# Optimization experiments

Hardware: AMD Instinct MI355X
Metric: run time of the kernel (lower is better)

Reference implementation:

```python
import jax, jax.numpy as jnp
import numpy as np

NUM_PROTOTYPES_PER_CLASS = 4
BATCH = 16384
NUM_CLASSES = 1000


def setup_inputs() -> dict:
    key = jax.random.key(0)
    k1, k2 = jax.random.split(key)
    batch_distances = jax.random.uniform(k1, (BATCH, NUM_CLASSES * NUM_PROTOTYPES_PER_CLASS), dtype=jnp.float32)
    labels = jax.random.randint(k2, (BATCH,), 0, NUM_CLASSES, dtype=jnp.int64)
    return {"batch_distances": batch_distances, "labels": labels}


def reference(batch_distances, labels):
    B, NP = batch_distances.shape
    P = NUM_PROTOTYPES_PER_CLASS
    C = NP // P
    # (B, C, P) -> soft-min over prototypes per class
    d = -jax.nn.logsumexp(-batch_distances.reshape(B, C, P), axis=2)  # (B, C)
    in_cls = jnp.take_along_axis(d, labels[:, None], axis=1)[:, 0]    # (B,)
    # leave-one-out mean over the other C-1 classes
    out_mean = (jnp.sum(d, axis=1) - in_cls) / (C - 1)                # (B,)
    loss = jnp.mean((in_cls * in_cls) / (out_mean * out_mean))
    return loss
```

## Files before the change

### kernel.cpp

```cpp
#include <hip/hip_runtime.h>

constexpr int BATCH   = 16384;
constexpr int NCLS    = 1000;
constexpr int PROTO   = 4;
constexpr int THREADS = 256;

__global__ __launch_bounds__(THREADS)
void mpl_row_kernel(const float* __restrict__ dist,
                    const int*   __restrict__ labels,
                    float*       __restrict__ terms) {
    const int row = blockIdx.x;
    const float4* __restrict__ rp =
        reinterpret_cast<const float4*>(dist + (size_t)row * (NCLS * PROTO));
    const int lab = labels[row];
    const int t   = threadIdx.x;

    float sum   = 0.0f;
    float incls = 0.0f;
    bool  have  = false;

    for (int c = t; c < NCLS; c += THREADS) {
        float4 v = rp[c];
        float m = fminf(fminf(v.x, v.y), fminf(v.z, v.w));
        float s = expf(m - v.x) + expf(m - v.y) + expf(m - v.z) + expf(m - v.w);
        float d = m - logf(s);
        sum += d;
        if (c == lab) { incls = d; have = true; }
    }

    #pragma unroll
    for (int off = 32; off; off >>= 1) sum += __shfl_down(sum, off, 64);

    __shared__ float s_wave[THREADS / 64];
    __shared__ float s_in;
    const int lane = t & 63, wid = t >> 6;
    if (lane == 0) s_wave[wid] = sum;
    if (have)      s_in = incls;
    __syncthreads();

    if (t == 0) {
        float total = s_wave[0] + s_wave[1] + s_wave[2] + s_wave[3];
        float ic    = s_in;
        float om    = (total - ic) * (1.0f / (NCLS - 1));
        terms[row]  = (ic * ic) / (om * om);
    }
}

__global__ __launch_bounds__(THREADS)
void mpl_reduce_kernel(const float* __restrict__ terms,
                       float*       __restrict__ out) {
    const int t = threadIdx.x;
    const float4* __restrict__ tp = reinterpret_cast<const float4*>(terms);
    float sum = 0.0f;
    for (int i = t; i < BATCH / 4; i += THREADS) {
        float4 v = tp[i];
        sum += (v.x + v.y) + (v.z + v.w);
    }
    #pragma unroll
    for (int off = 32; off; off >>= 1) sum += __shfl_down(sum, off, 64);

    __shared__ float s_wave[THREADS / 64];
    const int lane = t & 63, wid = t >> 6;
    if (lane == 0) s_wave[wid] = sum;
    __syncthreads();
    if (t == 0) {
        out[0] = (s_wave[0] + s_wave[1] + s_wave[2] + s_wave[3]) * (1.0f / BATCH);
    }
}

extern "C" void kernel_launch(void* const* d_in, const int* in_sizes, int n_in,
                              void* d_out, int out_size, void* d_ws, size_t ws_size,
                              hipStream_t stream) {
    const float* dist   = (const float*)d_in[0];
    const int*   labels = (const int*)d_in[1];
    float*       terms  = (float*)d_ws;
    float*       out    = (float*)d_out;

    mpl_row_kernel<<<BATCH, THREADS, 0, stream>>>(dist, labels, terms);
    mpl_reduce_kernel<<<1, THREADS, 0, stream>>>(terms, out);
}
```

Baseline: 355.1 us.

## Fuse row and reduce kernels with wave-per-row mapping and atomic final reduction

```diff
diff --git a/kernel.cpp b/kernel.cpp
--- a/kernel.cpp
+++ b/kernel.cpp
@@ -2,69 +2,64 @@
 
 constexpr int BATCH   = 16384;
 constexpr int NCLS    = 1000;
-constexpr int PROTO   = 4;
 constexpr int THREADS = 256;
+constexpr int BLOCKS  = 2048;
 
 __global__ __launch_bounds__(THREADS)
-void mpl_row_kernel(const float* __restrict__ dist,
-                    const int*   __restrict__ labels,
-                    float*       __restrict__ terms) {
-    const int row = blockIdx.x;
-    const float4* __restrict__ rp =
-        reinterpret_cast<const float4*>(dist + (size_t)row * (NCLS * PROTO));
-    const int lab = labels[row];
-    const int t   = threadIdx.x;
+void mpl_fused_kernel(const float* __restrict__ dist,
+                      const int*   __restrict__ labels,
+                      float*       __restrict__ acc,
+                      unsigned*    __restrict__ cnt,
+                      float*       __restrict__ out) {
+    const int t    = threadIdx.x;
+    const int lane = t & 63;
+    const int wid  = t >> 6;
+    const int gw   = blockIdx.x * 4 + wid;
 
-    float sum   = 0.0f;
-    float incls = 0.0f;
-    bool  have  = false;
+    float partial = 0.0f;
 
-    for (int c = t; c < NCLS; c += THREADS) {
-        float4 v = rp[c];
-        float m = fminf(fminf(v.x, v.y), fminf(v.z, v.w));
-        float s = expf(m - v.x) + expf(m - v.y) + expf(m - v.z) + expf(m - v.w);
-        float d = m - logf(s);
-        sum += d;
-        if (c == lab) { incls = d; have = true; }
+    for (int row = gw; row < BATCH; row += BLOCKS * 4) {
+        const float4* __restrict__ rp =
+            reinterpret_cast<const float4*>(dist + (size_t)row * (NCLS * 4));
+        const int lab = labels[row];
+
+        float sum = 0.0f, incls = 0.0f;
+        #pragma unroll
+        for (int it = 0; it < 16; ++it) {
+            const int c = it * 64 + lane;
+            if (c < NCLS) {
+                float4 v = rp[c];
+                float m = fminf(fminf(v.x, v.y), fminf(v.z, v.w));
+                float s = __expf(m - v.x) + __expf(m - v.y) +
+                          __expf(m - v.z) + __expf(m - v.w);
+                float d = m - __logf(s);
+                sum += d;
+                if (c == lab) incls = d;
+            }
+        }
+        #pragma unroll
+        for (int off = 32; off; off >>= 1) {
+            sum   += __shfl_xor(sum,   off, 64);
+            incls += __shfl_xor(incls, off, 64);
+        }
+        if (lane == 0) {
+            float om = (sum - incls) * (1.0f / (NCLS - 1));
+            partial += (incls * incls) / (om * om);
+        }
     }
 
-    #pragma unroll
-    for (int off = 32; off; off >>= 1) sum += __shfl_down(sum, off, 64);
-
-    __shared__ float s_wave[THREADS / 64];
-    __shared__ float s_in;
-    const int lane = t & 63, wid = t >> 6;
-    if (lane == 0) s_wave[wid] = sum;
-    if (have)      s_in = incls;
-    __syncthreads();
-
-    if (t == 0) {
-        float total = s_wave[0] + s_wave[1] + s_wave[2] + s_wave[3];
-        float ic    = s_in;
-        float om    = (total - ic) * (1.0f / (NCLS - 1));
-        terms[row]  = (ic * ic) / (om * om);
-    }
-}
-
-__global__ __launch_bounds__(THREADS)
-void mpl_reduce_kernel(const float* __restrict__ terms,
-                       float*       __restrict__ out) {
-    const int t = threadIdx.x;
-    const float4* __restrict__ tp = reinterpret_cast<const float4*>(terms);
-    float sum = 0.0f;
-    for (int i = t; i < BATCH / 4; i += THREADS) {
-        float4 v = tp[i];
-        sum += (v.x + v.y) + (v.z + v.w);
-    }
-    #pragma unroll
-    for (int off = 32; off; off >>= 1) sum += __shfl_down(sum, off, 64);
-
-    __shared__ float s_wave[THREADS / 64];
-    const int lane = t & 63, wid = t >> 6;
-    if (lane == 0) s_wave[wid] = sum;
+    __shared__ float s_p[4];
+    if (lane == 0) s_p[wid] = partial;
     __syncthreads();
     if (t == 0) {
-        out[0] = (s_wave[0] + s_wave[1] + s_wave[2] + s_wave[3]) * (1.0f / BATCH);
+        float blk = (s_p[0] + s_p[1]) + (s_p[2] + s_p[3]);
+        atomicAdd(acc, blk);
+        __threadfence();
+        unsigned done = atomicAdd(cnt, 1u);
+        if (done == gridDim.x - 1) {
+            float total = atomicAdd(acc, 0.0f);
+            out[0] = total * (1.0f / BATCH);
+        }
     }
 }
 
@@ -73,9 +68,10 @@
                               hipStream_t stream) {
     const float* dist   = (const float*)d_in[0];
     const int*   labels = (const int*)d_in[1];
-    float*       terms  = (float*)d_ws;
+    float*       acc    = (float*)d_ws;
+    unsigned*    cnt    = (unsigned*)d_ws + 1;
     float*       out    = (float*)d_out;
 
-    mpl_row_kernel<<<BATCH, THREADS, 0, stream>>>(dist, labels, terms);
-    mpl_reduce_kernel<<<1, THREADS, 0, stream>>>(terms, out);
+    hipMemsetAsync(d_ws, 0, 8, stream);
+    mpl_fused_kernel<<<BLOCKS, THREADS, 0, stream>>>(dist, labels, acc, cnt, out);
 }
```

After: 446.8 us. 1.26x slower.
